# Kernel tuning notes

Measured on AMD Instinct MI355X. Metric: run time of the kernel, lower is better.

The kernel has to match this reference:

```python
import jax, jax.numpy as jnp
import numpy as np

ALPHA = 300.0  # attractor strength (exp variant: exp(-alpha*|dx|^gamma)*dx, gamma=2)


def setup_inputs() -> dict:
    key = jax.random.key(0)
    k0, k1, k2, k3 = jax.random.split(key, 4)
    n, c, h, w = 4, 256, 128, 128
    mlp_dim, n_attractors, n_bins = 128, 16, 64
    x = jax.random.normal(k0, (n, c, h, w), jnp.float32)
    b_prev = jax.random.uniform(k1, (n, n_bins, h, w), jnp.float32)  # bin centers
    w1 = jax.random.normal(k2, (mlp_dim, c), jnp.float32) * 0.02
    b1 = jnp.zeros((mlp_dim,), jnp.float32)
    w2 = jax.random.normal(k3, (n_attractors, mlp_dim), jnp.float32) * 0.02
    b2 = jnp.zeros((n_attractors,), jnp.float32)
    return {"x": x, "b_prev": b_prev, "w1": w1, "b1": b1, "w2": w2, "b2": b2}


def reference(x, b_prev, w1, b1, w2, b2):
    # 1x1 conv MLP head: Conv2d(c->mlp) -> ReLU -> Conv2d(mlp->n_attractors) -> Softplus
    hfeat = jax.nn.relu(jnp.einsum('nchw,oc->nohw', x, w1) + b1[None, :, None, None])
    A = jax.nn.softplus(jnp.einsum('nchw,oc->nohw', hfeat, w2) + b2[None, :, None, None])
    # b_prev interpolated to (h, w) == identity here (same spatial size)
    b_centers = b_prev
    # dx: [n, n_attractors, n_bins, h, w]
    dx = A[:, :, None, :, :] - b_centers[:, None, :, :, :]
    # exp attractor with gamma=2: exp(-alpha*dx^2) * dx, summed over attractors ('sum' kind)
    delta_c = jnp.sum(jnp.exp(-ALPHA * dx * dx) * dx, axis=1)
    b_new_centers = b_centers + delta_c
    return (b_new_centers, b_new_centers)
```

## Files before the change

kernel.cpp:

```cpp
#include <hip/hip_runtime.h>
#include <hip/hip_bf16.h>
#include <stdint.h>


#define HW 16384
#define ALPHA 300.0f

typedef short bf16x8_t __attribute__((ext_vector_type(8)));
typedef float f32x4_t __attribute__((ext_vector_type(4)));
typedef unsigned int u32x4_t __attribute__((ext_vector_type(4)));

__device__ __forceinline__ unsigned short f2bf(float f) {
  unsigned int u = __builtin_bit_cast(unsigned int, f);
  u += 0x7fffu + ((u >> 16) & 1u);
  return (unsigned short)(u >> 16);
}
__device__ __forceinline__ unsigned int pack2(float a, float b) {
  return (unsigned int)f2bf(a) | ((unsigned int)f2bf(b) << 16);
}

__global__ void zoed_prep(const float* __restrict__ w1,
                          const float* __restrict__ w2,
                          unsigned short* __restrict__ blob) {
  int i = blockIdx.x * 256 + threadIdx.x;
  if (i < 32768) {
    int o = i >> 8, c = i & 255;
    float v = w1[i];
    int idx = (c >> 5) * 4096 + o * 32 + ((((c >> 3) & 3) ^ (o & 3)) << 3) + (c & 7);
    blob[idx] = f2bf(v);
  } else {
    int i2 = i - 32768;
    int a = i2 >> 7, o = i2 & 127;
    float v = w2[i2];
    int idx = 32768 + (o >> 5) * 512 + a * 32 + ((((o >> 3) & 3) ^ (a & 3)) << 3) + (o & 7);
    blob[idx] = f2bf(v);
  }
}

__global__ __launch_bounds__(256, 4) void zoed_fused(
    const float* __restrict__ x, const float* __restrict__ bprev,
    const float* __restrict__ b1, const float* __restrict__ b2,
    const unsigned short* __restrict__ wblob, float* __restrict__ out) {
  __shared__ __align__(16) char smem[24576];
  char* xbuf = smem;
  char* w1buf = smem + 4096;
  char* hid = smem;
  char* Albuf = smem + 16384;
  char* w2buf = smem + 20480;

  const int t = threadIdx.x;
  const int lane = t & 63;
  const int l15 = lane & 15;
  const int quad = lane >> 4;
  const int wv = t >> 6;
  const int wm = wv & 1;
  const int wn = wv >> 1;
  const int sw = ((quad ^ (lane & 3)) << 4);

  const int blk = blockIdx.x;
  const int n = blk >> 8;
  const int p0 = (blk & 255) << 6;

  *(u32x4_t*)(w2buf + t * 16) =
      *(const u32x4_t*)((const char*)wblob + 65536 + t * 16);

  f32x4_t acc[4][2];
#pragma unroll
  for (int i = 0; i < 4; i++)
#pragma unroll
    for (int j = 0; j < 2; j++) acc[i][j] = (f32x4_t){0.f, 0.f, 0.f, 0.f};

  const int sp = t & 63;
  const int sg = t >> 6;

  const float* xsbase = x + (size_t)(n * 256 + sg * 8) * HW + p0 + sp;
  float xf0, xf1, xf2, xf3, xf4, xf5, xf6, xf7;
  u32x4_t wfa, wfb;
  {
    const float* xs = xsbase;
    xf0 = xs[0 * HW]; xf1 = xs[1 * HW]; xf2 = xs[2 * HW]; xf3 = xs[3 * HW];
    xf4 = xs[4 * HW]; xf5 = xs[5 * HW]; xf6 = xs[6 * HW]; xf7 = xs[7 * HW];
    const char* wsrc = (const char*)wblob + t * 32;
    wfa = *(const u32x4_t*)wsrc;
    wfb = *(const u32x4_t*)(wsrc + 16);
  }

  for (int kb = 0; kb < 8; ++kb) {
    __syncthreads();
    {
      u32x4_t v = {pack2(xf0, xf1), pack2(xf2, xf3), pack2(xf4, xf5),
                   pack2(xf6, xf7)};
      *(u32x4_t*)(xbuf + sp * 64 + ((sg ^ (sp & 3)) << 4)) = v;
      *(u32x4_t*)(w1buf + t * 32) = wfa;
      *(u32x4_t*)(w1buf + t * 32 + 16) = wfb;
    }
    __syncthreads();
    if (kb < 7) {
      const float* xs = xsbase + (size_t)((kb + 1) * 32) * HW;
      xf0 = xs[0 * HW]; xf1 = xs[1 * HW]; xf2 = xs[2 * HW]; xf3 = xs[3 * HW];
      xf4 = xs[4 * HW]; xf5 = xs[5 * HW]; xf6 = xs[6 * HW]; xf7 = xs[7 * HW];
      const char* wsrc = (const char*)wblob + (kb + 1) * 8192 + t * 32;
      wfa = *(const u32x4_t*)wsrc;
      wfb = *(const u32x4_t*)(wsrc + 16);
    }
    bf16x8_t af[4], bfm[2];
#pragma unroll
    for (int tm = 0; tm < 4; tm++)
      af[tm] = *(const bf16x8_t*)(w1buf + (wm * 64 + tm * 16 + l15) * 64 + sw);
#pragma unroll
    for (int tn = 0; tn < 2; tn++)
      bfm[tn] = *(const bf16x8_t*)(xbuf + (wn * 32 + tn * 16 + l15) * 64 + sw);
#pragma unroll
    for (int tm = 0; tm < 4; tm++)
#pragma unroll
      for (int tn = 0; tn < 2; tn++)
        acc[tm][tn] = __builtin_amdgcn_mfma_f32_16x16x32_bf16(
            af[tm], bfm[tn], acc[tm][tn], 0, 0, 0);
  }

  __syncthreads();
#pragma unroll
  for (int tm = 0; tm < 4; tm++) {
    f32x4_t b1v = *(const f32x4_t*)(b1 + wm * 64 + tm * 16 + quad * 4);
    int kc = wm * 2 + (tm >> 1);
    int g = (tm & 1) * 2 + (quad >> 1);
    int off8 = (quad & 1) * 8;
#pragma unroll
    for (int tn = 0; tn < 2; tn++) {
      f32x4_t h = acc[tm][tn] + b1v;
      h[0] = fmaxf(h[0], 0.f);
      h[1] = fmaxf(h[1], 0.f);
      h[2] = fmaxf(h[2], 0.f);
      h[3] = fmaxf(h[3], 0.f);
      int prow = wn * 32 + tn * 16 + l15;
      unsigned int* dst = (unsigned int*)(hid + kc * 4096 + prow * 64 +
                                          ((g ^ (prow & 3)) << 4) + off8);
      dst[0] = pack2(h[0], h[1]);
      dst[1] = pack2(h[2], h[3]);
    }
  }
  __syncthreads();
  {
    f32x4_t acc2 = (f32x4_t){0.f, 0.f, 0.f, 0.f};
    const int prow = wv * 16 + l15;
#pragma unroll
    for (int kc = 0; kc < 4; kc++) {
      bf16x8_t a2 = *(const bf16x8_t*)(w2buf + kc * 1024 + l15 * 64 + sw);
      bf16x8_t bh = *(const bf16x8_t*)(hid + kc * 4096 + prow * 64 + sw);
      acc2 = __builtin_amdgcn_mfma_f32_16x16x32_bf16(a2, bh, acc2, 0, 0, 0);
    }
    f32x4_t b2v = *(const f32x4_t*)(b2 + quad * 4);
    f32x4_t z = acc2 + b2v;
    f32x4_t spv;
#pragma unroll
    for (int r = 0; r < 4; r++) {
      float zz = z[r];
      spv[r] = fmaxf(zz, 0.f) + log1pf(__expf(-fabsf(zz)));
    }
    *(f32x4_t*)(Albuf + prow * 64 + ((quad ^ (prow & 3)) << 4)) = spv;
  }
  __syncthreads();
  {
    const int p = t & 63;
    const int grp = t >> 6;
    float Av[16];
#pragma unroll
    for (int q = 0; q < 4; q++) {
      f32x4_t v = *(const f32x4_t*)(Albuf + p * 64 + ((q ^ (p & 3)) << 4));
      Av[q * 4 + 0] = v[0];
      Av[q * 4 + 1] = v[1];
      Av[q * 4 + 2] = v[2];
      Av[q * 4 + 3] = v[3];
    }
    size_t base = (size_t)n * 64 * HW + (size_t)(grp * 16) * HW + (size_t)(p0 + p);
    const float* bp = bprev + base;
    float* o1 = out + base;
    float* o2 = out + (size_t)4 * 64 * HW + base;
#pragma unroll 4
    for (int b = 0; b < 16; b++) {
      float c = bp[(size_t)b * HW];
      float d0 = 0.f, d1 = 0.f;
#pragma unroll
      for (int a = 0; a < 8; a++) {
        float dx = Av[a] - c;
        float e = __expf(dx * dx * -ALPHA);
        d0 = fmaf(e, dx, d0);
      }
#pragma unroll
      for (int a = 8; a < 16; a++) {
        float dx = Av[a] - c;
        float e = __expf(dx * dx * -ALPHA);
        d1 = fmaf(e, dx, d1);
      }
      float r = c + (d0 + d1);
      __builtin_nontemporal_store(r, o1 + (size_t)b * HW);
      __builtin_nontemporal_store(r, o2 + (size_t)b * HW);
    }
  }
}

extern "C" void kernel_launch(void* const* d_in, const int* in_sizes, int n_in,
                              void* d_out, int out_size, void* d_ws,
                              size_t ws_size, hipStream_t stream) {
  const float* x = (const float*)d_in[0];
  const float* bprev = (const float*)d_in[1];
  const float* w1 = (const float*)d_in[2];
  const float* b1 = (const float*)d_in[3];
  const float* w2 = (const float*)d_in[4];
  const float* b2 = (const float*)d_in[5];
  float* outp = (float*)d_out;
  unsigned short* blob = (unsigned short*)d_ws;

  zoed_prep<<<136, 256, 0, stream>>>(w1, w2, blob);
  zoed_fused<<<1024, 256, 0, stream>>>(x, bprev, b1, b2, blob, outp);
}
```

Before: 136.8 us.

## Load W1 fragments directly to registers and double-buffer x tile

The W1 A-fragments are now read straight from the pre-swizzled global blob into registers, prefetched one k-block ahead, instead of being staged through LDS. The x tile is double-buffered in shared memory, so each k-step needs only one barrier instead of two, and x loads are issued four k-blocks deep. The b_prev values and W2 fragments are also loaded into registers before the hidden-layer epilogue so their latency overlaps the MLP work. The cost is much higher register pressure (32 floats of x, 16 b_prev values, extra fragments), which can lower occupancy below the launch bound target or cause spills.

Measured after the change: 133.9 us. -2.1%, faster.

```diff
diff --git a/kernel.cpp b/kernel.cpp
--- a/kernel.cpp
+++ b/kernel.cpp
@@ -41,12 +41,9 @@
     const float* __restrict__ x, const float* __restrict__ bprev,
     const float* __restrict__ b1, const float* __restrict__ b2,
     const unsigned short* __restrict__ wblob, float* __restrict__ out) {
-  __shared__ __align__(16) char smem[24576];
-  char* xbuf = smem;
-  char* w1buf = smem + 4096;
+  __shared__ __align__(16) char smem[20480];
   char* hid = smem;
   char* Albuf = smem + 16384;
-  char* w2buf = smem + 20480;
 
   const int t = threadIdx.x;
   const int lane = t & 63;
@@ -61,62 +58,77 @@
   const int n = blk >> 8;
   const int p0 = (blk & 255) << 6;
 
-  *(u32x4_t*)(w2buf + t * 16) =
-      *(const u32x4_t*)((const char*)wblob + 65536 + t * 16);
-
-  f32x4_t acc[4][2];
-#pragma unroll
-  for (int i = 0; i < 4; i++)
-#pragma unroll
-    for (int j = 0; j < 2; j++) acc[i][j] = (f32x4_t){0.f, 0.f, 0.f, 0.f};
-
   const int sp = t & 63;
   const int sg = t >> 6;
 
   const float* xsbase = x + (size_t)(n * 256 + sg * 8) * HW + p0 + sp;
-  float xf0, xf1, xf2, xf3, xf4, xf5, xf6, xf7;
-  u32x4_t wfa, wfb;
-  {
-    const float* xs = xsbase;
-    xf0 = xs[0 * HW]; xf1 = xs[1 * HW]; xf2 = xs[2 * HW]; xf3 = xs[3 * HW];
-    xf4 = xs[4 * HW]; xf5 = xs[5 * HW]; xf6 = xs[6 * HW]; xf7 = xs[7 * HW];
-    const char* wsrc = (const char*)wblob + t * 32;
-    wfa = *(const u32x4_t*)wsrc;
-    wfb = *(const u32x4_t*)(wsrc + 16);
-  }
-
+  float xr[4][8];
+#pragma unroll
+  for (int c = 0; c < 4; c++)
+#pragma unroll
+    for (int j = 0; j < 8; j++)
+      xr[c][j] = xsbase[(size_t)(c * 32 + j) * HW];
+
+  const char* wbase = (const char*)wblob + (wm * 64 + l15) * 64 + sw;
+  bf16x8_t afn[4];
+#pragma unroll
+  for (int tm = 0; tm < 4; tm++)
+    afn[tm] = *(const bf16x8_t*)(wbase + tm * 1024);
+
+  f32x4_t acc[4][2];
+#pragma unroll
+  for (int i = 0; i < 4; i++)
+#pragma unroll
+    for (int j = 0; j < 2; j++) acc[i][j] = (f32x4_t){0.f, 0.f, 0.f, 0.f};
+
+#pragma unroll
   for (int kb = 0; kb < 8; ++kb) {
+    char* xb = smem + (kb & 1) * 4096;
+    bf16x8_t afc[4];
+#pragma unroll
+    for (int tm = 0; tm < 4; tm++) afc[tm] = afn[tm];
+    if (kb < 7) {
+#pragma unroll
+      for (int tm = 0; tm < 4; tm++)
+        afn[tm] = *(const bf16x8_t*)(wbase + (kb + 1) * 8192 + tm * 1024);
+    }
+    {
+      u32x4_t v = {pack2(xr[kb & 3][0], xr[kb & 3][1]),
+                   pack2(xr[kb & 3][2], xr[kb & 3][3]),
+                   pack2(xr[kb & 3][4], xr[kb & 3][5]),
+                   pack2(xr[kb & 3][6], xr[kb & 3][7])};
+      *(u32x4_t*)(xb + sp * 64 + ((sg ^ (sp & 3)) << 4)) = v;
+    }
+    if (kb < 4) {
+#pragma unroll
+      for (int j = 0; j < 8; j++)
+        xr[kb & 3][j] = xsbase[(size_t)((kb + 4) * 32 + j) * HW];
+    }
     __syncthreads();
-    {
-      u32x4_t v = {pack2(xf0, xf1), pack2(xf2, xf3), pack2(xf4, xf5),
-                   pack2(xf6, xf7)};
-      *(u32x4_t*)(xbuf + sp * 64 + ((sg ^ (sp & 3)) << 4)) = v;
-      *(u32x4_t*)(w1buf + t * 32) = wfa;
-      *(u32x4_t*)(w1buf + t * 32 + 16) = wfb;
-    }
-    __syncthreads();
-    if (kb < 7) {
-      const float* xs = xsbase + (size_t)((kb + 1) * 32) * HW;
-      xf0 = xs[0 * HW]; xf1 = xs[1 * HW]; xf2 = xs[2 * HW]; xf3 = xs[3 * HW];
-      xf4 = xs[4 * HW]; xf5 = xs[5 * HW]; xf6 = xs[6 * HW]; xf7 = xs[7 * HW];
-      const char* wsrc = (const char*)wblob + (kb + 1) * 8192 + t * 32;
-      wfa = *(const u32x4_t*)wsrc;
-      wfb = *(const u32x4_t*)(wsrc + 16);
-    }
-    bf16x8_t af[4], bfm[2];
-#pragma unroll
-    for (int tm = 0; tm < 4; tm++)
-      af[tm] = *(const bf16x8_t*)(w1buf + (wm * 64 + tm * 16 + l15) * 64 + sw);
+    bf16x8_t bfm[2];
 #pragma unroll
     for (int tn = 0; tn < 2; tn++)
-      bfm[tn] = *(const bf16x8_t*)(xbuf + (wn * 32 + tn * 16 + l15) * 64 + sw);
+      bfm[tn] = *(const bf16x8_t*)(xb + (wn * 32 + tn * 16 + l15) * 64 + sw);
 #pragma unroll
     for (int tm = 0; tm < 4; tm++)
 #pragma unroll
       for (int tn = 0; tn < 2; tn++)
         acc[tm][tn] = __builtin_amdgcn_mfma_f32_16x16x32_bf16(
-            af[tm], bfm[tn], acc[tm][tn], 0, 0, 0);
-  }
+            afc[tm], bfm[tn], acc[tm][tn], 0, 0, 0);
+  }
+
+  const int ap = t & 63;
+  const int grp = t >> 6;
+  size_t obase = (size_t)n * 64 * HW + (size_t)(grp * 16) * HW + (size_t)(p0 + ap);
+  const float* bp = bprev + obase;
+  float bpr[16];
+#pragma unroll
+  for (int b = 0; b < 16; b++) bpr[b] = bp[(size_t)b * HW];
+  bf16x8_t a2[4];
+#pragma unroll
+  for (int kc = 0; kc < 4; kc++)
+    a2[kc] = *(const bf16x8_t*)((const char*)wblob + 65536 + kc * 1024 +
+                                l15 * 64 + sw);
 
   __syncthreads();
 #pragma unroll
@@ -145,9 +157,8 @@
     const int prow = wv * 16 + l15;
 #pragma unroll
     for (int kc = 0; kc < 4; kc++) {
-      bf16x8_t a2 = *(const bf16x8_t*)(w2buf + kc * 1024 + l15 * 64 + sw);
       bf16x8_t bh = *(const bf16x8_t*)(hid + kc * 4096 + prow * 64 + sw);
-      acc2 = __builtin_amdgcn_mfma_f32_16x16x32_bf16(a2, bh, acc2, 0, 0, 0);
+      acc2 = __builtin_amdgcn_mfma_f32_16x16x32_bf16(a2[kc], bh, acc2, 0, 0, 0);
     }
     f32x4_t b2v = *(const f32x4_t*)(b2 + quad * 4);
     f32x4_t z = acc2 + b2v;
@@ -161,24 +172,20 @@
   }
   __syncthreads();
   {
-    const int p = t & 63;
-    const int grp = t >> 6;
     float Av[16];
 #pragma unroll
     for (int q = 0; q < 4; q++) {
-      f32x4_t v = *(const f32x4_t*)(Albuf + p * 64 + ((q ^ (p & 3)) << 4));
+      f32x4_t v = *(const f32x4_t*)(Albuf + ap * 64 + ((q ^ (ap & 3)) << 4));
       Av[q * 4 + 0] = v[0];
       Av[q * 4 + 1] = v[1];
       Av[q * 4 + 2] = v[2];
       Av[q * 4 + 3] = v[3];
     }
-    size_t base = (size_t)n * 64 * HW + (size_t)(grp * 16) * HW + (size_t)(p0 + p);
-    const float* bp = bprev + base;
-    float* o1 = out + base;
-    float* o2 = out + (size_t)4 * 64 * HW + base;
-#pragma unroll 4
+    float* o1 = out + obase;
+    float* o2 = out + (size_t)4 * 64 * HW + obase;
+#pragma unroll
     for (int b = 0; b < 16; b++) {
-      float c = bp[(size_t)b * HW];
+      float c = bpr[b];
       float d0 = 0.f, d1 = 0.f;
 #pragma unroll
       for (int a = 0; a < 8; a++) {
```
